# Kernel optimization log

Hardware: AMD Instinct MI355X
Metric: run time of the kernel (lower is better)

## Reference

```python
import jax, jax.numpy as jnp
import numpy as np

N_NODES = 100000
N_EDGES = 1600000
F_IN, HIDDEN, N_CLASS, K = 64, 64, 32, 3
DROPOUT_P = 0.5


def setup_inputs() -> dict:
    key = jax.random.key(0)
    ks = jax.random.split(key, 5)
    x = jax.random.normal(ks[0], (N_NODES, F_IN), dtype=jnp.float32)
    edge_index = jax.random.randint(ks[1], (2, N_EDGES), 0, N_NODES, dtype=jnp.int64)
    W1 = jax.random.normal(ks[2], (K, F_IN, HIDDEN), dtype=jnp.float32) * (1.0 / np.sqrt(F_IN))
    b1 = jnp.zeros((HIDDEN,), dtype=jnp.float32)
    W2 = jax.random.normal(ks[3], (K, HIDDEN, N_CLASS), dtype=jnp.float32) * (1.0 / np.sqrt(HIDDEN))
    b2 = jnp.zeros((N_CLASS,), dtype=jnp.float32)
    return {"x": x, "edge_index": edge_index, "W1": W1, "b1": b1, "W2": W2, "b2": b2}


def _cheb_norm(edge_index, n_nodes):
    # PyG ChebConv sym norm with lambda_max=2: L_hat = -D^{-1/2} A D^{-1/2}
    row, col = edge_index[0], edge_index[1]
    deg = jax.ops.segment_sum(jnp.ones_like(row, dtype=jnp.float32), row, num_segments=n_nodes)
    dinv = jnp.where(deg > 0, jax.lax.rsqrt(jnp.maximum(deg, 1.0)), 0.0)
    return -(dinv[row] * dinv[col])  # [E]


def _cheb_conv(x, row, col, norm, W, b):
    # Chebyshev recursion: Tx0=x, Tx1=L_hat x, Tx_k = 2 L_hat Tx_{k-1} - Tx_{k-2}
    def prop(h):
        return jax.ops.segment_sum(norm[:, None] * h[col], row, num_segments=h.shape[0])
    Tx0 = x
    out = Tx0 @ W[0]
    Tx1 = prop(Tx0)
    out = out + Tx1 @ W[1]
    for k in range(2, W.shape[0]):
        Tx2 = 2.0 * prop(Tx1) - Tx0
        out = out + Tx2 @ W[k]
        Tx0, Tx1 = Tx1, Tx2
    return out + b


def reference(x, edge_index, W1, b1, W2, b2):
    row, col = edge_index[0], edge_index[1]
    norm = _cheb_norm(edge_index, x.shape[0])
    h = jax.nn.relu(_cheb_conv(x, row, col, norm, W1, b1))
    # dropout (training=True) with fixed key, inverted scaling
    keep = jax.random.bernoulli(jax.random.key(42), 1.0 - DROPOUT_P, h.shape)
    h = jnp.where(keep, h / (1.0 - DROPOUT_P), 0.0)
    out = _cheb_conv(h, row, col, norm, W2, b2)
    return jax.nn.log_softmax(out, axis=-1)
```

## Files before the change

### kernel.cpp

```cpp
#include <hip/hip_runtime.h>


static constexpr int BLK = 256;
static constexpr int SCAN_CHUNK = 256;
static constexpr int ROWB = 256;
static constexpr int RB_SHIFT = 8;
static constexpr int BCAP = 6144;
static constexpr int CHUNK = 8192;

typedef _Float16 f16x8 __attribute__((ext_vector_type(8)));
typedef _Float16 f16x2 __attribute__((ext_vector_type(2)));
typedef float f32x4 __attribute__((ext_vector_type(4)));

__device__ __forceinline__ unsigned rotl32(unsigned x, int r) {
    return (x << r) | (x >> (32 - r));
}

__device__ __forceinline__ unsigned tf_word(unsigned i) {
    const unsigned ks0 = 0u;
    const unsigned ks1 = 42u;
    const unsigned ks2 = 0u ^ 42u ^ 0x1BD11BDAu;
    unsigned x0 = 0u + ks0;
    unsigned x1 = i + ks1;
#define TF_RND(r) { x0 += x1; x1 = rotl32(x1, (r)); x1 ^= x0; }
    TF_RND(13) TF_RND(15) TF_RND(26) TF_RND(6)
    x0 += ks1; x1 += ks2 + 1u;
    TF_RND(17) TF_RND(29) TF_RND(16) TF_RND(24)
    x0 += ks2; x1 += ks0 + 2u;
    TF_RND(13) TF_RND(15) TF_RND(26) TF_RND(6)
    x0 += ks0; x1 += ks1 + 3u;
    TF_RND(17) TF_RND(29) TF_RND(16) TF_RND(24)
    x0 += ks1; x1 += ks2 + 4u;
    TF_RND(13) TF_RND(15) TF_RND(26) TF_RND(6)
    x0 += ks2; x1 += ks0 + 5u;
#undef TF_RND
    return x0 ^ x1;
}

__device__ __forceinline__ unsigned short f2h(float f) {
    union { _Float16 h; unsigned short u; } c; c.h = (_Float16)f; return c.u;
}
__device__ __forceinline__ unsigned pack2h(float a, float b) {
    union { f16x2 h; unsigned u; } c;
    c.h[0] = (_Float16)a; c.h[1] = (_Float16)b;
    return c.u;
}

__global__ void k_detect(const int* __restrict__ ei, int* __restrict__ flags) {
    __shared__ int cnt_nz;
    int t = threadIdx.x;
    if (t == 0) cnt_nz = 0;
    __syncthreads();
    if (ei[2 * t + 1] != 0) atomicAdd(&cnt_nz, 1);
    __syncthreads();
    if (t == 0) flags[0] = (cnt_nz == 0) ? 1 : 0;
}

__global__ void __launch_bounds__(256) k_drop(int NW, unsigned long long* __restrict__ dmask) {
    int idx = blockIdx.x * 256 + threadIdx.x;
    unsigned word = (idx < NW) ? tf_word((unsigned)idx) : 0u;
    unsigned long long bal = __ballot(word >> 31);
    if ((threadIdx.x & 63) == 0 && idx < NW) dmask[idx >> 6] = bal;
}

__global__ void __launch_bounds__(256) k_bin(const int* __restrict__ ei, int E,
                                             const int* __restrict__ flags,
                                             int* __restrict__ bcnt,
                                             unsigned* __restrict__ bdata, int NB) {
    __shared__ unsigned sval[CHUNK];
    __shared__ unsigned short sbkt[CHUNK];
    __shared__ int h[512], ex[512], cur[512], basep[512];
    int t = threadIdx.x;
    int start = blockIdx.x * CHUNK;
    int lim = min(CHUNK, E - start);
    bool i64 = flags[0] != 0;
    h[t] = 0; h[t + 256] = 0;
    __syncthreads();
    unsigned vv[32];
    unsigned short bb_[32];
#pragma unroll
    for (int k = 0; k < 32; ++k) {
        int idx = k * 256 + t;
        int e = start + idx;
        if (idx < lim) {
            int r, c;
            if (i64) { r = ei[2 * e]; c = ei[2 * (E + e)]; }
            else     { r = ei[e];     c = ei[E + e]; }
            int b = r >> RB_SHIFT;
            vv[k] = ((unsigned)(r & (ROWB - 1)) << 17) | (unsigned)c;
            bb_[k] = (unsigned short)b;
            atomicAdd(&h[b], 1);
        } else {
            bb_[k] = 0xFFFF;
        }
    }
    __syncthreads();
    int i0 = t, i1 = t + 256;
    ex[i0] = h[i0]; ex[i1] = h[i1];
    __syncthreads();
    for (int off = 1; off < 512; off <<= 1) {
        int v0 = (i0 >= off) ? ex[i0 - off] : 0;
        int v1 = (i1 >= off) ? ex[i1 - off] : 0;
        __syncthreads();
        ex[i0] += v0; ex[i1] += v1;
        __syncthreads();
    }
    int e0 = ex[i0] - h[i0], e1 = ex[i1] - h[i1];
    __syncthreads();
    ex[i0] = e0; cur[i0] = e0;
    ex[i1] = e1; cur[i1] = e1;
    if (i0 < NB && h[i0] > 0) basep[i0] = atomicAdd(&bcnt[i0], h[i0]);
    if (i1 < NB && h[i1] > 0) basep[i1] = atomicAdd(&bcnt[i1], h[i1]);
    __syncthreads();
#pragma unroll
    for (int k = 0; k < 32; ++k) {
        if (bb_[k] != 0xFFFF) {
            int p = atomicAdd(&cur[bb_[k]], 1);
            sval[p] = vv[k];
            sbkt[p] = bb_[k];
        }
    }
    __syncthreads();
    for (int i = t; i < lim; i += 256) {
        int b = sbkt[i];
        int gpos = basep[b] + (i - ex[b]);
        if (gpos < BCAP) bdata[(size_t)b * BCAP + gpos] = sval[i];
    }
}

__global__ void __launch_bounds__(256) k_hist2(const unsigned* __restrict__ bdata,
                                               const int* __restrict__ bcnt,
                                               int N, int* __restrict__ deg,
                                               float* __restrict__ dinv) {
    __shared__ int h[ROWB];
    int t = threadIdx.x, b = blockIdx.x;
    h[t] = 0;
    __syncthreads();
    int cnt = min(bcnt[b], BCAP);
    for (int i = t; i < cnt; i += 256)
        atomicAdd(&h[bdata[(size_t)b * BCAP + i] >> 17], 1);
    __syncthreads();
    int r = b * ROWB + t;
    if (r < N) {
        int d = h[t];
        deg[r] = d;
        dinv[r] = (d > 0) ? rsqrtf((float)d) : 0.0f;
    }
}

__global__ void k_scanA(const int* __restrict__ deg, int N, int* __restrict__ blk_sum) {
    __shared__ int lds[SCAN_CHUNK];
    int i = blockIdx.x * SCAN_CHUNK + threadIdx.x;
    int v = (i < N) ? deg[i] : 0;
    lds[threadIdx.x] = v;
    __syncthreads();
    for (int off = SCAN_CHUNK / 2; off > 0; off >>= 1) {
        if (threadIdx.x < off) lds[threadIdx.x] += lds[threadIdx.x + off];
        __syncthreads();
    }
    if (threadIdx.x == 0) blk_sum[blockIdx.x] = lds[0];
}

__global__ void k_scanB(int* __restrict__ blk_sum, int nb) {
    __shared__ int lds[1024];
    int t = threadIdx.x;
    int v = (t < nb) ? blk_sum[t] : 0;
    lds[t] = v;
    __syncthreads();
    for (int off = 1; off < 1024; off <<= 1) {
        int val = (t >= off) ? lds[t - off] : 0;
        __syncthreads();
        lds[t] += val;
        __syncthreads();
    }
    if (t < nb) blk_sum[t] = lds[t] - v;
}

__global__ void k_scanC(const int* __restrict__ deg, int N, int E,
                        const int* __restrict__ blk_sum, int* __restrict__ row_ptr) {
    __shared__ int lds[SCAN_CHUNK];
    int t = threadIdx.x;
    int i = blockIdx.x * SCAN_CHUNK + t;
    int v = (i < N) ? deg[i] : 0;
    lds[t] = v;
    __syncthreads();
    for (int off = 1; off < SCAN_CHUNK; off <<= 1) {
        int val = (t >= off) ? lds[t - off] : 0;
        __syncthreads();
        lds[t] += val;
        __syncthreads();
    }
    if (i < N) row_ptr[i] = blk_sum[blockIdx.x] + lds[t] - v;
    if (blockIdx.x == gridDim.x - 1 && t == SCAN_CHUNK - 1) row_ptr[N] = E;
}

__global__ void __launch_bounds__(256) k_place(const unsigned* __restrict__ bdata,
                                               const int* __restrict__ bcnt,
                                               const int* __restrict__ row_ptr,
                                               int N, int* __restrict__ sdst) {
    __shared__ int cur[ROWB];
    __shared__ int staged[BCAP];
    int t = threadIdx.x, b = blockIdx.x;
    int r0 = b * ROWB;
    int rbase = row_ptr[r0];
    int r = r0 + t;
    cur[t] = (r < N) ? (row_ptr[r] - rbase) : 0;
    __syncthreads();
    int cnt = min(bcnt[b], BCAP);
    for (int i = t; i < cnt; i += 256) {
        unsigned val = bdata[(size_t)b * BCAP + i];
        int p = atomicAdd(&cur[val >> 17], 1);
        staged[p] = (int)(val & 0x1FFFFu);
    }
    __syncthreads();
    for (int i = t; i < cnt; i += 256) sdst[rbase + i] = staged[i];
}

__global__ void k_wprep(const float* __restrict__ W1, const float* __restrict__ W2,
                        unsigned short* __restrict__ wt1,
                        unsigned short* __restrict__ wt2) {
    int idx = blockIdx.x * 256 + threadIdx.x;
    if (idx < 12288) {
        int c = idx >> 6, r6 = idx & 63;
        int slot = (r6 >> 3) ^ (c & 7);
        int k = slot * 8 + (r6 & 7);
        float v;
        if (c < 64)       v = W1[k * 64 + c] - W1[8192 + k * 64 + c];
        else if (c < 128) v = W1[4096 + k * 64 + (c - 64)];
        else              v = W1[8192 + k * 64 + (c - 128)];
        wt1[idx] = f2h(v);
    } else {
        int j = idx - 12288;
        int c = j >> 6, r6 = j & 63;
        int slot = (r6 >> 3) ^ (c & 7);
        int k = slot * 8 + (r6 & 7);
        float v;
        if (c < 32)      v = W2[k * 32 + c] - W2[4096 + k * 32 + c];
        else if (c < 64) v = W2[2048 + k * 32 + (c - 32)];
        else             v = W2[4096 + k * 32 + (c - 64)];
        wt2[j] = f2h(v);
    }
}

__global__ void __launch_bounds__(512) k_dense3(const float* __restrict__ x,
                                                const unsigned short* __restrict__ wt1,
                                                const float* __restrict__ b1,
                                                const float* __restrict__ dinv,
                                                int N,
                                                unsigned short* __restrict__ B16,
                                                unsigned short* __restrict__ C16,
                                                unsigned short* __restrict__ D16) {
    __shared__ unsigned short lds[20480] __attribute__((aligned(16)));
    __shared__ float sb[64];
    int t = threadIdx.x;
    int v0 = blockIdx.x * 128;
    {
        const uint4* src = (const uint4*)wt1;
        uint4* dst = (uint4*)&lds[8192];
        for (int i = t; i < 1536; i += 512) dst[i] = src[i];
    }
    if (t < 64) sb[t] = b1[t];
    {
        int row = t >> 2, c0 = (t & 3) << 4;
        int v = min(v0 + row, N - 1);
        const float* xp = x + (size_t)v * 64 + c0;
        float4 f0 = *(const float4*)xp;
        float4 f1 = *(const float4*)(xp + 4);
        float4 f2 = *(const float4*)(xp + 8);
        float4 f3 = *(const float4*)(xp + 12);
        int key = row & 7;
        int s0 = c0 >> 3;
        f16x8 h0, h1;
        h0[0] = (_Float16)f0.x; h0[1] = (_Float16)f0.y;
        h0[2] = (_Float16)f0.z; h0[3] = (_Float16)f0.w;
        h0[4] = (_Float16)f1.x; h0[5] = (_Float16)f1.y;
        h0[6] = (_Float16)f1.z; h0[7] = (_Float16)f1.w;
        h1[0] = (_Float16)f2.x; h1[1] = (_Float16)f2.y;
        h1[2] = (_Float16)f2.z; h1[3] = (_Float16)f2.w;
        h1[4] = (_Float16)f3.x; h1[5] = (_Float16)f3.y;
        h1[6] = (_Float16)f3.z; h1[7] = (_Float16)f3.w;
        *(f16x8*)&lds[row * 64 + ((s0 ^ key) << 3)] = h0;
        *(f16x8*)&lds[row * 64 + (((s0 + 1) ^ key) << 3)] = h1;
    }
    __syncthreads();

    int w = t >> 6, l = t & 63;
    int lr = l & 15, lk = l >> 4;
    int key = lr & 7;
    int arow = w * 16 + lr;
    f16x8 a0 = *(const f16x8*)&lds[arow * 64 + (((0 + lk) ^ key) << 3)];
    f16x8 a1 = *(const f16x8*)&lds[arow * 64 + (((4 + lk) ^ key) << 3)];
    f32x4 acc[12];
#pragma unroll
    for (int i = 0; i < 12; ++i) acc[i] = (f32x4){0.0f, 0.0f, 0.0f, 0.0f};
#pragma unroll
    for (int nt = 0; nt < 12; ++nt) {
        int bc = nt * 16 + lr;
        const unsigned short* wb = &lds[8192 + bc * 64];
        f16x8 b0 = *(const f16x8*)&wb[((0 + lk) ^ key) << 3];
        f16x8 b1v = *(const f16x8*)&wb[((4 + lk) ^ key) << 3];
        acc[nt] = __builtin_amdgcn_mfma_f32_16x16x32_f16(a0, b0, acc[nt], 0, 0, 0);
        acc[nt] = __builtin_amdgcn_mfma_f32_16x16x32_f16(a1, b1v, acc[nt], 0, 0, 0);
    }
    float4 dv4 = *(const float4*)&dinv[v0 + w * 16 + lk * 4];
    float dsc[4] = {dv4.x, dv4.y, dv4.z, dv4.w};
    __syncthreads();
#pragma unroll
    for (int nt = 0; nt < 4; ++nt) {
        int col = nt * 16 + lr;
        float bv = sb[col];
#pragma unroll
        for (int r = 0; r < 4; ++r) {
            int vloc = w * 16 + lk * 4 + r;
            lds[vloc * 64 + col] = f2h(acc[nt][r] + bv);
        }
    }
    __syncthreads();
#pragma unroll
    for (int q = 0; q < 2; ++q) {
        int i = q * 512 + t;
        int row = i >> 3, ch = i & 7;
        int v = v0 + row;
        if (v < N) *(uint4*)(D16 + (size_t)v * 64 + ch * 8) = ((const uint4*)lds)[i];
    }
    __syncthreads();
#pragma unroll
    for (int nt = 4; nt < 8; ++nt) {
        int col = (nt - 4) * 16 + lr;
#pragma unroll
        for (int r = 0; r < 4; ++r) {
            int vloc = w * 16 + lk * 4 + r;
            lds[vloc * 128 + col] = f2h(acc[nt][r]);
        }
    }
#pragma unroll
    for (int nt = 8; nt < 12; ++nt) {
        int col = (nt - 4) * 16 + lr;
#pragma unroll
        for (int r = 0; r < 4; ++r) {
            int vloc = w * 16 + lk * 4 + r;
            lds[vloc * 128 + col] = f2h(acc[nt][r] * dsc[r]);
        }
    }
    __syncthreads();
#pragma unroll
    for (int q = 0; q < 4; ++q) {
        int i = q * 512 + t;
        int row = i >> 4, ch = i & 15;
        int v = v0 + row;
        if (v < N) {
            uint4 val = *(const uint4*)&lds[i * 8];
            unsigned short* dst = (ch < 8)
                ? (B16 + (size_t)v * 64 + ch * 8)
                : (C16 + (size_t)v * 64 + (ch - 8) * 8);
            *(uint4*)dst = val;
        }
    }
}

__global__ void __launch_bounds__(512) k_dense3b(const unsigned short* __restrict__ wt2,
                                                 const float* __restrict__ dinv,
                                                 int N,
                                                 unsigned short* __restrict__ B16,
                                                 const unsigned short* __restrict__ C16h,
                                                 float* __restrict__ P0,
                                                 unsigned short* __restrict__ P1h) {
    __shared__ unsigned short lds[14336] __attribute__((aligned(16)));
    int t = threadIdx.x;
    int v0 = blockIdx.x * 128;
    {
        const uint4* src = (const uint4*)wt2;
        uint4* dst = (uint4*)&lds[8192];
        for (int i = t; i < 768; i += 512) dst[i] = src[i];
    }
    {
        int row = t >> 2, s0 = (t & 3) * 2;
        int v = min(v0 + row, N - 1);
        const uint4* cp = (const uint4*)(C16h + (size_t)v * 64);
        uint4 u0 = cp[s0];
        uint4 u1 = cp[s0 + 1];
        int key = row & 7;
        *(uint4*)&lds[row * 64 + ((s0 ^ key) << 3)] = u0;
        *(uint4*)&lds[row * 64 + (((s0 + 1) ^ key) << 3)] = u1;
    }
    __syncthreads();

    int w = t >> 6, l = t & 63;
    int lr = l & 15, lk = l >> 4;
    int key = lr & 7;
    int arow = w * 16 + lr;
    f16x8 a0 = *(const f16x8*)&lds[arow * 64 + (((0 + lk) ^ key) << 3)];
    f16x8 a1 = *(const f16x8*)&lds[arow * 64 + (((4 + lk) ^ key) << 3)];
    f32x4 acc[6];
#pragma unroll
    for (int i = 0; i < 6; ++i) acc[i] = (f32x4){0.0f, 0.0f, 0.0f, 0.0f};
#pragma unroll
    for (int nt = 0; nt < 6; ++nt) {
        int bc = nt * 16 + lr;
        const unsigned short* wb = &lds[8192 + bc * 64];
        f16x8 b0 = *(const f16x8*)&wb[((0 + lk) ^ key) << 3];
        f16x8 b1v = *(const f16x8*)&wb[((4 + lk) ^ key) << 3];
        acc[nt] = __builtin_amdgcn_mfma_f32_16x16x32_f16(a0, b0, acc[nt], 0, 0, 0);
        acc[nt] = __builtin_amdgcn_mfma_f32_16x16x32_f16(a1, b1v, acc[nt], 0, 0, 0);
    }
    float4 dv4 = *(const float4*)&dinv[v0 + w * 16 + lk * 4];
    float dsc[4] = {dv4.x, dv4.y, dv4.z, dv4.w};
#pragma unroll
    for (int nt = 0; nt < 2; ++nt) {
        int col = nt * 16 + lr;
#pragma unroll
        for (int r = 0; r < 4; ++r) {
            int v = v0 + w * 16 + lk * 4 + r;
            if (v < N) P0[(size_t)v * 32 + col] = acc[nt][r];
        }
    }
    __syncthreads();
#pragma unroll
    for (int nt = 2; nt < 4; ++nt) {
        int col = (nt - 2) * 16 + lr;
#pragma unroll
        for (int r = 0; r < 4; ++r) {
            int vloc = w * 16 + lk * 4 + r;
            lds[vloc * 64 + col] = f2h(acc[nt][r]);
        }
    }
#pragma unroll
    for (int nt = 4; nt < 6; ++nt) {
        int col = (nt - 2) * 16 + lr;
#pragma unroll
        for (int r = 0; r < 4; ++r) {
            int vloc = w * 16 + lk * 4 + r;
            lds[vloc * 64 + col] = f2h(acc[nt][r] * dsc[r]);
        }
    }
    __syncthreads();
#pragma unroll
    for (int q = 0; q < 2; ++q) {
        int i = q * 512 + t;
        int row = i >> 3, ch = i & 7;
        int v = v0 + row;
        if (v < N) {
            uint4 val = ((const uint4*)lds)[i];
            unsigned short* dst = (ch < 4)
                ? (P1h + (size_t)v * 32 + ch * 8)
                : (B16 + (size_t)v * 32 + (ch - 4) * 8);
            *(uint4*)dst = val;
        }
    }
}

template <int PITCH>
__device__ __forceinline__ void gatherH(const unsigned short* __restrict__ src,
                                        const int* __restrict__ sdst,
                                        int beg, int end, int grp, int fl,
                                        float a[8]) {
    constexpr int NG = 32 / (PITCH / 8);
    f16x8 acc;
#pragma unroll
    for (int q = 0; q < 8; ++q) acc[q] = (_Float16)0;
    int e = beg + grp;
    for (; e + NG < end; e += 2 * NG) {
        int c0 = sdst[e];
        int c1 = sdst[e + NG];
        f16x8 r0 = *(const f16x8*)(src + (size_t)c0 * PITCH + 8 * fl);
        f16x8 r1 = *(const f16x8*)(src + (size_t)c1 * PITCH + 8 * fl);
        acc = acc + r0;
        acc = acc + r1;
    }
    if (e < end) {
        int c = sdst[e];
        f16x8 r = *(const f16x8*)(src + (size_t)c * PITCH + 8 * fl);
        acc = acc + r;
    }
#pragma unroll
    for (int m = PITCH / 8; m < 32; m <<= 1) {
        union { f16x8 h; int i4[4]; } u;
        u.h = acc;
#pragma unroll
        for (int q = 0; q < 4; ++q) u.i4[q] = __shfl_xor(u.i4[q], m);
        acc = acc + u.h;
    }
#pragma unroll
    for (int q = 0; q < 8; ++q) a[q] = (float)acc[q];
}

__global__ void __launch_bounds__(BLK) k_gath1(const unsigned short* __restrict__ C16,
                                               unsigned short* __restrict__ B16,
                                               const float* __restrict__ dinv,
                                               const int* __restrict__ row_ptr,
                                               const int* __restrict__ sdst,
                                               int N) {
    int v = blockIdx.x * 8 + (threadIdx.x >> 5);
    if (v >= N) return;
    int hl = threadIdx.x & 31;
    int grp = hl >> 3, fl = hl & 7;
    float a[8];
    gatherH<64>(C16, sdst, row_ptr[v], row_ptr[v + 1], grp, fl, a);
    if (grp == 0) {
        float di = dinv[v];
        float dv = -2.0f * di;
        unsigned short* p = B16 + (size_t)v * 64 + 8 * fl;
        f16x8 b = *(const f16x8*)p;
        uint4 o;
        o.x = pack2h(di * fmaf(dv, a[0], (float)b[0]), di * fmaf(dv, a[1], (float)b[1]));
        o.y = pack2h(di * fmaf(dv, a[2], (float)b[2]), di * fmaf(dv, a[3], (float)b[3]));
        o.z = pack2h(di * fmaf(dv, a[4], (float)b[4]), di * fmaf(dv, a[5], (float)b[5]));
        o.w = pack2h(di * fmaf(dv, a[6], (float)b[6]), di * fmaf(dv, a[7], (float)b[7]));
        *(uint4*)p = o;
    }
}

__global__ void __launch_bounds__(BLK) k_gath2(const unsigned short* __restrict__ D16,
                                               const unsigned short* __restrict__ B16,
                                               unsigned short* __restrict__ C16h,
                                               const unsigned long long* __restrict__ dmask,
                                               const float* __restrict__ dinv,
                                               const int* __restrict__ row_ptr,
                                               const int* __restrict__ sdst,
                                               int N) {
    int v = blockIdx.x * 8 + (threadIdx.x >> 5);
    if (v >= N) return;
    int hl = threadIdx.x & 31;
    int grp = hl >> 3, fl = hl & 7;
    float a[8];
    gatherH<64>(B16, sdst, row_ptr[v], row_ptr[v + 1], grp, fl, a);
    if (grp == 0) {
        unsigned long long dm = dmask[v] >> (8 * fl);
        float dv = -dinv[v];
        f16x8 d = *(const f16x8*)(D16 + (size_t)v * 64 + 8 * fl);
        float o[8];
#pragma unroll
        for (int k = 0; k < 8; ++k)
            o[k] = fmaxf(fmaf(dv, a[k], (float)d[k]), 0.0f);
#pragma unroll
        for (int k = 0; k < 8; ++k)
            o[k] = ((dm >> k) & 1ull) ? 0.0f : o[k] * 2.0f;
        uint4 oo;
        oo.x = pack2h(o[0], o[1]); oo.y = pack2h(o[2], o[3]);
        oo.z = pack2h(o[4], o[5]); oo.w = pack2h(o[6], o[7]);
        *(uint4*)(C16h + (size_t)v * 64 + 8 * fl) = oo;
    }
}

__global__ void __launch_bounds__(BLK) k_gath3(const unsigned short* __restrict__ B16,
                                               const unsigned short* __restrict__ P1h,
                                               unsigned short* __restrict__ R16,
                                               const float* __restrict__ dinv,
                                               const int* __restrict__ row_ptr,
                                               const int* __restrict__ sdst,
                                               int N) {
    int v = blockIdx.x * 8 + (threadIdx.x >> 5);
    if (v >= N) return;
    int hl = threadIdx.x & 31;
    int grp = hl >> 2, fl = hl & 3;
    float a[8];
    gatherH<32>(B16, sdst, row_ptr[v], row_ptr[v + 1], grp, fl, a);
    if (grp == 0) {
        float di = dinv[v];
        float dv = -2.0f * di;
        f16x8 d = *(const f16x8*)(P1h + (size_t)v * 32 + 8 * fl);
        uint4 o;
        o.x = pack2h(di * fmaf(dv, a[0], (float)d[0]), di * fmaf(dv, a[1], (float)d[1]));
        o.y = pack2h(di * fmaf(dv, a[2], (float)d[2]), di * fmaf(dv, a[3], (float)d[3]));
        o.z = pack2h(di * fmaf(dv, a[4], (float)d[4]), di * fmaf(dv, a[5], (float)d[5]));
        o.w = pack2h(di * fmaf(dv, a[6], (float)d[6]), di * fmaf(dv, a[7], (float)d[7]));
        *(uint4*)(R16 + (size_t)v * 32 + 8 * fl) = o;
    }
}

__global__ void __launch_bounds__(BLK) k_gath4(const unsigned short* __restrict__ R16,
                                               const float* __restrict__ P0,
                                               const float* __restrict__ dinv,
                                               const int* __restrict__ row_ptr,
                                               const int* __restrict__ sdst,
                                               const float* __restrict__ b2,
                                               int N, float* __restrict__ out) {
    int v = blockIdx.x * 8 + (threadIdx.x >> 5);
    if (v >= N) return;
    int hl = threadIdx.x & 31;
    int grp = hl >> 2, fl = hl & 3;
    float a[8];
    gatherH<32>(R16, sdst, row_ptr[v], row_ptr[v + 1], grp, fl, a);
    float dv = -dinv[v];
    const float* dp = P0 + (size_t)v * 32 + 8 * fl;
    float4 dA = *(const float4*)dp;
    float4 dB = *(const float4*)(dp + 4);
    const float* bp = b2 + 8 * fl;
    float4 bA = *(const float4*)bp;
    float4 bB = *(const float4*)(bp + 4);
    float o[8];
    o[0] = fmaf(dv, a[0], dA.x + bA.x);
    o[1] = fmaf(dv, a[1], dA.y + bA.y);
    o[2] = fmaf(dv, a[2], dA.z + bA.z);
    o[3] = fmaf(dv, a[3], dA.w + bA.w);
    o[4] = fmaf(dv, a[4], dB.x + bB.x);
    o[5] = fmaf(dv, a[5], dB.y + bB.y);
    o[6] = fmaf(dv, a[6], dB.z + bB.z);
    o[7] = fmaf(dv, a[7], dB.w + bB.w);
    float m = o[0];
#pragma unroll
    for (int k = 1; k < 8; ++k) m = fmaxf(m, o[k]);
    m = fmaxf(m, __shfl_xor(m, 1));
    m = fmaxf(m, __shfl_xor(m, 2));
    float s = 0.0f;
#pragma unroll
    for (int k = 0; k < 8; ++k) s += __expf(o[k] - m);
    s += __shfl_xor(s, 1);
    s += __shfl_xor(s, 2);
    float lse = m + __logf(s);
    if (grp == 0) {
        float* op = out + (size_t)v * 32 + 8 * fl;
        *(float4*)op = make_float4(o[0] - lse, o[1] - lse, o[2] - lse, o[3] - lse);
        *(float4*)(op + 4) = make_float4(o[4] - lse, o[5] - lse, o[6] - lse, o[7] - lse);
    }
}

extern "C" void kernel_launch(void* const* d_in, const int* in_sizes, int n_in,
                              void* d_out, int out_size, void* d_ws, size_t ws_size,
                              hipStream_t stream) {
    const float* x  = (const float*)d_in[0];
    const int* ei   = (const int*)d_in[1];
    const float* W1 = (const float*)d_in[2];
    const float* b1 = (const float*)d_in[3];
    const float* W2 = (const float*)d_in[4];
    const float* b2 = (const float*)d_in[5];
    float* out = (float*)d_out;

    const int N = in_sizes[0] / 64;
    const int E = in_sizes[1] / 2;
    const int NB = (N + ROWB - 1) >> RB_SHIFT;

    char* ws = (char*)d_ws;
    size_t off = 0;
    auto alloc = [&](size_t bytes) -> void* {
        void* p = ws + off;
        off = (off + bytes + 511) & ~(size_t)511;
        return p;
    };
    int*      flags   = (int*)alloc(16);
    int*      deg     = (int*)alloc((size_t)N * 4);
    float*    dinv    = (float*)alloc((size_t)N * 4);
    int*      row_ptr = (int*)alloc(((size_t)N + 1) * 4);
    int*      blk_sum = (int*)alloc(4096);
    int*      bcnt    = (int*)alloc((size_t)NB * 4);
    size_t dbytes = (size_t)N * 64 * 4;
    size_t bdbytes = (size_t)NB * BCAP * 4;
    unsigned* bdata = (unsigned*)alloc(dbytes > bdbytes ? dbytes : bdbytes);
    unsigned short* D16 = (unsigned short*)bdata;
    float*    P0    = (float*)bdata;
    unsigned short* P1h = (unsigned short*)((char*)bdata + (size_t)N * 32 * 4);
    int*      sdst  = (int*)alloc((size_t)E * 4);
    unsigned short* C16h = (unsigned short*)alloc((size_t)N * 64 * 2);
    unsigned short* B16 = (unsigned short*)alloc((size_t)N * 64 * 2);
    unsigned short* C16 = (unsigned short*)alloc((size_t)N * 64 * 2);
    unsigned short* R16 = C16;
    unsigned long long* dmask = (unsigned long long*)alloc((size_t)N * 8);
    unsigned short* wt1 = (unsigned short*)alloc(12288 * 2);
    unsigned short* wt2 = (unsigned short*)alloc(6144 * 2);

    hipMemsetAsync(bcnt, 0, (size_t)NB * 4, stream);

    const int gW8 = (N + 7) / 8;
    const int gDM = (N + 127) / 128;
    const int nb = (N + SCAN_CHUNK - 1) / SCAN_CHUNK;
    const int gBin = (E + CHUNK - 1) / CHUNK;
    const int gDrop = (N * 64 + 255) / 256;

    k_wprep<<<72, 256, 0, stream>>>(W1, W2, wt1, wt2);
    k_drop<<<gDrop, 256, 0, stream>>>(N * 64, dmask);
    k_detect<<<1, 256, 0, stream>>>(ei, flags);
    k_bin<<<gBin, 256, 0, stream>>>(ei, E, flags, bcnt, bdata, NB);
    k_hist2<<<NB, 256, 0, stream>>>(bdata, bcnt, N, deg, dinv);
    k_scanA<<<nb, SCAN_CHUNK, 0, stream>>>(deg, N, blk_sum);
    k_scanB<<<1, 1024, 0, stream>>>(blk_sum, nb);
    k_scanC<<<nb, SCAN_CHUNK, 0, stream>>>(deg, N, E, blk_sum, row_ptr);
    k_place<<<NB, 256, 0, stream>>>(bdata, bcnt, row_ptr, N, sdst);

    k_dense3<<<gDM, 512, 0, stream>>>(x, wt1, b1, dinv, N, B16, C16, D16);
    k_gath1<<<gW8, BLK, 0, stream>>>(C16, B16, dinv, row_ptr, sdst, N);
    k_gath2<<<gW8, BLK, 0, stream>>>(D16, B16, C16h, dmask, dinv, row_ptr, sdst, N);

    k_dense3b<<<gDM, 512, 0, stream>>>(wt2, dinv, N, B16, C16h, P0, P1h);
    k_gath3<<<gW8, BLK, 0, stream>>>(B16, P1h, R16, dinv, row_ptr, sdst, N);
    k_gath4<<<gW8, BLK, 0, stream>>>(R16, P0, dinv, row_ptr, sdst, b2, N, out);
}
```

Baseline: 284.7 us.

## Shrink lanes per node in gather kernels, unroll by four, fold detect into drop

The gather kernels now give each destination node 16 lanes (64-wide features) or 8 lanes (32-wide) instead of 32. Fewer lanes means fewer edge groups per node, so each lane walks more edges, and the inner loop is unrolled to four loads in flight. With about 16 edges per node on average, this aims to cut idle lanes and shuffle-reduction overhead and pack more nodes into each block. The single-block edge-index dtype detection is merged into the dropout-mask kernel as an extra block to save a launch. The trade-off is longer serial edge chains for high-degree nodes, and f16 accumulation now runs over more terms per lane.

```diff
diff --git a/kernel.cpp b/kernel.cpp
--- a/kernel.cpp
+++ b/kernel.cpp
@@ -46,17 +46,19 @@
     return c.u;
 }
 
-__global__ void k_detect(const int* __restrict__ ei, int* __restrict__ flags) {
-    __shared__ int cnt_nz;
-    int t = threadIdx.x;
-    if (t == 0) cnt_nz = 0;
-    __syncthreads();
-    if (ei[2 * t + 1] != 0) atomicAdd(&cnt_nz, 1);
-    __syncthreads();
-    if (t == 0) flags[0] = (cnt_nz == 0) ? 1 : 0;
-}
-
-__global__ void __launch_bounds__(256) k_drop(int NW, unsigned long long* __restrict__ dmask) {
+__global__ void __launch_bounds__(256) k_drop(int NW, const int* __restrict__ ei,
+                                              int* __restrict__ flags,
+                                              unsigned long long* __restrict__ dmask) {
+    if (blockIdx.x == gridDim.x - 1) {
+        __shared__ int cnt_nz;
+        int t = threadIdx.x;
+        if (t == 0) cnt_nz = 0;
+        __syncthreads();
+        if (ei[2 * t + 1] != 0) atomicAdd(&cnt_nz, 1);
+        __syncthreads();
+        if (t == 0) flags[0] = (cnt_nz == 0) ? 1 : 0;
+        return;
+    }
     int idx = blockIdx.x * 256 + threadIdx.x;
     unsigned word = (idx < NW) ? tf_word((unsigned)idx) : 0u;
     unsigned long long bal = __ballot(word >> 31);
@@ -449,31 +451,37 @@
     }
 }
 
-template <int PITCH>
+template <int PITCH, int LPN>
 __device__ __forceinline__ void gatherH(const unsigned short* __restrict__ src,
                                         const int* __restrict__ sdst,
                                         int beg, int end, int grp, int fl,
                                         float a[8]) {
-    constexpr int NG = 32 / (PITCH / 8);
+    constexpr int NG = LPN / (PITCH / 8);
     f16x8 acc;
 #pragma unroll
     for (int q = 0; q < 8; ++q) acc[q] = (_Float16)0;
     int e = beg + grp;
-    for (; e + NG < end; e += 2 * NG) {
+    for (; e + 3 * NG < end; e += 4 * NG) {
         int c0 = sdst[e];
         int c1 = sdst[e + NG];
+        int c2 = sdst[e + 2 * NG];
+        int c3 = sdst[e + 3 * NG];
         f16x8 r0 = *(const f16x8*)(src + (size_t)c0 * PITCH + 8 * fl);
         f16x8 r1 = *(const f16x8*)(src + (size_t)c1 * PITCH + 8 * fl);
+        f16x8 r2 = *(const f16x8*)(src + (size_t)c2 * PITCH + 8 * fl);
+        f16x8 r3 = *(const f16x8*)(src + (size_t)c3 * PITCH + 8 * fl);
         acc = acc + r0;
         acc = acc + r1;
-    }
-    if (e < end) {
+        acc = acc + r2;
+        acc = acc + r3;
+    }
+    for (; e < end; e += NG) {
         int c = sdst[e];
         f16x8 r = *(const f16x8*)(src + (size_t)c * PITCH + 8 * fl);
         acc = acc + r;
     }
 #pragma unroll
-    for (int m = PITCH / 8; m < 32; m <<= 1) {
+    for (int m = PITCH / 8; m < LPN; m <<= 1) {
         union { f16x8 h; int i4[4]; } u;
         u.h = acc;
 #pragma unroll
@@ -490,12 +498,12 @@
                                                const int* __restrict__ row_ptr,
                                                const int* __restrict__ sdst,
                                                int N) {
-    int v = blockIdx.x * 8 + (threadIdx.x >> 5);
+    int v = blockIdx.x * 16 + (threadIdx.x >> 4);
     if (v >= N) return;
-    int hl = threadIdx.x & 31;
-    int grp = hl >> 3, fl = hl & 7;
+    int ln = threadIdx.x & 15;
+    int grp = ln >> 3, fl = ln & 7;
     float a[8];
-    gatherH<64>(C16, sdst, row_ptr[v], row_ptr[v + 1], grp, fl, a);
+    gatherH<64, 16>(C16, sdst, row_ptr[v], row_ptr[v + 1], grp, fl, a);
     if (grp == 0) {
         float di = dinv[v];
         float dv = -2.0f * di;
@@ -518,12 +526,12 @@
                                                const int* __restrict__ row_ptr,
                                                const int* __restrict__ sdst,
                                                int N) {
-    int v = blockIdx.x * 8 + (threadIdx.x >> 5);
+    int v = blockIdx.x * 16 + (threadIdx.x >> 4);
     if (v >= N) return;
-    int hl = threadIdx.x & 31;
-    int grp = hl >> 3, fl = hl & 7;
+    int ln = threadIdx.x & 15;
+    int grp = ln >> 3, fl = ln & 7;
     float a[8];
-    gatherH<64>(B16, sdst, row_ptr[v], row_ptr[v + 1], grp, fl, a);
+    gatherH<64, 16>(B16, sdst, row_ptr[v], row_ptr[v + 1], grp, fl, a);
     if (grp == 0) {
         unsigned long long dm = dmask[v] >> (8 * fl);
         float dv = -dinv[v];
@@ -549,12 +557,12 @@
                                                const int* __restrict__ row_ptr,
                                                const int* __restrict__ sdst,
                                                int N) {
-    int v = blockIdx.x * 8 + (threadIdx.x >> 5);
+    int v = blockIdx.x * 32 + (threadIdx.x >> 3);
     if (v >= N) return;
-    int hl = threadIdx.x & 31;
-    int grp = hl >> 2, fl = hl & 3;
+    int ln = threadIdx.x & 7;
+    int grp = ln >> 2, fl = ln & 3;
     float a[8];
-    gatherH<32>(B16, sdst, row_ptr[v], row_ptr[v + 1], grp, fl, a);
+    gatherH<32, 8>(B16, sdst, row_ptr[v], row_ptr[v + 1], grp, fl, a);
     if (grp == 0) {
         float di = dinv[v];
         float dv = -2.0f * di;
@@ -575,12 +583,12 @@
                                                const int* __restrict__ sdst,
                                                const float* __restrict__ b2,
                                                int N, float* __restrict__ out) {
-    int v = blockIdx.x * 8 + (threadIdx.x >> 5);
+    int v = blockIdx.x * 32 + (threadIdx.x >> 3);
     if (v >= N) return;
-    int hl = threadIdx.x & 31;
-    int grp = hl >> 2, fl = hl & 3;
+    int ln = threadIdx.x & 7;
+    int grp = ln >> 2, fl = ln & 3;
     float a[8];
-    gatherH<32>(R16, sdst, row_ptr[v], row_ptr[v + 1], grp, fl, a);
+    gatherH<32, 8>(R16, sdst, row_ptr[v], row_ptr[v + 1], grp, fl, a);
     float dv = -dinv[v];
     const float* dp = P0 + (size_t)v * 32 + 8 * fl;
     float4 dA = *(const float4*)dp;
@@ -660,15 +668,15 @@
 
     hipMemsetAsync(bcnt, 0, (size_t)NB * 4, stream);
 
-    const int gW8 = (N + 7) / 8;
+    const int gW16 = (N + 15) / 16;
+    const int gW32 = (N + 31) / 32;
     const int gDM = (N + 127) / 128;
     const int nb = (N + SCAN_CHUNK - 1) / SCAN_CHUNK;
     const int gBin = (E + CHUNK - 1) / CHUNK;
     const int gDrop = (N * 64 + 255) / 256;
 
     k_wprep<<<72, 256, 0, stream>>>(W1, W2, wt1, wt2);
-    k_drop<<<gDrop, 256, 0, stream>>>(N * 64, dmask);
-    k_detect<<<1, 256, 0, stream>>>(ei, flags);
+    k_drop<<<gDrop + 1, 256, 0, stream>>>(N * 64, ei, flags, dmask);
     k_bin<<<gBin, 256, 0, stream>>>(ei, E, flags, bcnt, bdata, NB);
     k_hist2<<<NB, 256, 0, stream>>>(bdata, bcnt, N, deg, dinv);
     k_scanA<<<nb, SCAN_CHUNK, 0, stream>>>(deg, N, blk_sum);
@@ -677,10 +685,10 @@
     k_place<<<NB, 256, 0, stream>>>(bdata, bcnt, row_ptr, N, sdst);
 
     k_dense3<<<gDM, 512, 0, stream>>>(x, wt1, b1, dinv, N, B16, C16, D16);
-    k_gath1<<<gW8, BLK, 0, stream>>>(C16, B16, dinv, row_ptr, sdst, N);
-    k_gath2<<<gW8, BLK, 0, stream>>>(D16, B16, C16h, dmask, dinv, row_ptr, sdst, N);
+    k_gath1<<<gW16, BLK, 0, stream>>>(C16, B16, dinv, row_ptr, sdst, N);
+    k_gath2<<<gW16, BLK, 0, stream>>>(D16, B16, C16h, dmask, dinv, row_ptr, sdst, N);
 
     k_dense3b<<<gDM, 512, 0, stream>>>(wt2, dinv, N, B16, C16h, P0, P1h);
-    k_gath3<<<gW8, BLK, 0, stream>>>(B16, P1h, R16, dinv, row_ptr, sdst, N);
-    k_gath4<<<gW8, BLK, 0, stream>>>(R16, P0, dinv, row_ptr, sdst, b2, N, out);
-}
+    k_gath3<<<gW32, BLK, 0, stream>>>(B16, P1h, R16, dinv, row_ptr, sdst, N);
+    k_gath4<<<gW32, BLK, 0, stream>>>(R16, P0, dinv, row_ptr, sdst, b2, N, out);
+}
```

Result: faster. 274.7 us (-3.5%).
